# Performance work log

Hardware: AMD Instinct MI355X
Metric: run time of the kernel (lower is better)

Reference implementation:

```python
import jax, jax.numpy as jnp
import numpy as np

B, T, D = 2, 2048, 2048
N, K, H = 16, 8, 128  # heads, kv heads, head_dim
F = 8192              # ffn hidden


def _apply_rope(x, positions, max_wavelength=10000):
    # x: [B, L, heads, H]; positions: [B, L]
    half = x.shape[-1] // 2
    freq_exponents = (2.0 / x.shape[-1]) * jnp.arange(half, dtype=jnp.float32)
    timescale = max_wavelength ** freq_exponents
    radians = positions.astype(jnp.float32)[..., None] / timescale[None, None, :]
    radians = radians[..., None, :]  # [B, L, 1, half]
    sin, cos = jnp.sin(radians), jnp.cos(radians)
    x1, x2 = jnp.split(x, 2, axis=-1)
    return jnp.concatenate([x1 * cos - x2 * sin, x2 * cos + x1 * sin], axis=-1)


def _rms_norm(x, scale):
    var = jnp.mean(jnp.square(x), axis=-1, keepdims=True)
    return x * jax.lax.rsqrt(var + 1e-6) * (1 + scale)


def setup_inputs() -> dict:
    key = jax.random.key(0)
    ks = jax.random.split(key, 8)
    s = 0.02
    x = jax.random.normal(ks[0], (B, T, D), jnp.float32)
    positions = jnp.broadcast_to(jnp.arange(T, dtype=jnp.int32)[None, :], (B, T))
    causal = jnp.tril(jnp.ones((T, T), dtype=bool))
    attn_mask = jnp.broadcast_to(causal[None, None, :, :], (B, 1, T, T))
    return {
        "x": x,
        "positions": positions,
        "attn_mask": attn_mask,
        "w_q": jax.random.normal(ks[1], (N, D, H), jnp.float32) * s,
        "w_kv": jax.random.normal(ks[2], (2, K, D, H), jnp.float32) * s,
        "w_attn_vec": jax.random.normal(ks[3], (N, H, D), jnp.float32) * s,
        "scale_pre_attn": jax.random.normal(ks[4], (D,), jnp.float32) * s,
        "scale_pre_ffw": jax.random.normal(ks[5], (D,), jnp.float32) * s,
        "w_gating": jax.random.normal(ks[6], (2, D, F), jnp.float32) * s,
        "w_linear": jax.random.normal(ks[7], (F, D), jnp.float32) * s,
    }


def reference(x, positions, attn_mask, w_q, w_kv, w_attn_vec,
              scale_pre_attn, scale_pre_ffw, w_gating, w_linear):
    # pre-attention RMSNorm
    xn = _rms_norm(x, scale_pre_attn)

    # GQA projections
    q = jnp.einsum('BTD,NDH->BTNH', xn, w_q)
    kv = jnp.einsum('BSD,eKDH->eBSKH', xn, w_kv)
    k, v = kv[0], kv[1]

    q = _apply_rope(q, positions) * (H ** -0.5)
    k = _apply_rope(k, positions)

    G = N // K
    q = q.reshape(q.shape[0], q.shape[1], K, G, H)  # B T K G H
    logits = jnp.einsum('BTKGH,BSKH->BKGTS', q, k).astype(jnp.float32)
    big_neg = -2.3819763e38
    masked = jnp.where(attn_mask[:, :, None, :, :], logits, big_neg)
    probs = jax.nn.softmax(masked, axis=-1).astype(k.dtype)
    enc = jnp.einsum('BKGTS,BSKH->BTKGH', probs, v)
    enc = enc.reshape(enc.shape[0], enc.shape[1], N, H)
    attn_out = jnp.einsum('BTNH,NHD->BTD', enc, w_attn_vec)

    # residual + pre-FFN RMSNorm + GeGLU FFN
    residual = x + attn_out
    h = _rms_norm(residual, scale_pre_ffw)
    gate = jax.nn.gelu(jnp.dot(h, w_gating[0]))
    act = gate * jnp.dot(h, w_gating[1])
    out = residual + jnp.dot(act, w_linear)
    return out
```

## Files before the change

### kernel.cpp

```cpp
#include <hip/hip_runtime.h>
#include <hip/hip_bf16.h>


typedef __attribute__((ext_vector_type(8))) short bf16x8;
typedef __attribute__((ext_vector_type(4))) float f32x4;

#define GLP(p) ((const __attribute__((address_space(1))) void*)(p))
#define LDSP(p) ((__attribute__((address_space(3))) void*)(p))
#define FBAR() do { asm volatile("" ::: "memory"); __builtin_amdgcn_s_barrier(); asm volatile("" ::: "memory"); } while (0)

__device__ __forceinline__ float bf2f(unsigned short h) {
  union { unsigned int u; float f; } v; v.u = ((unsigned int)h) << 16; return v.f;
}
__device__ __forceinline__ unsigned short f2bf(float f) {
  union { float f; unsigned int u; } v; v.f = f;
  unsigned int r = v.u + 0x7fffu + ((v.u >> 16) & 1u);
  return (unsigned short)(r >> 16);
}
__device__ __forceinline__ float gelu_f(float x) {
  float t = tanhf(0.7978845608028654f * (x + 0.044715f * x * x * x));
  return 0.5f * x * (1.f + t);
}

template <int IN_F32>
__global__ __launch_bounds__(256) void rmsnorm_kernel(const void* __restrict__ x_,
                                                      const float* __restrict__ scale,
                                                      unsigned short* __restrict__ out) {
  int row = blockIdx.x, tid = threadIdx.x;
  float f[8]; float ss = 0.f;
  if (IN_F32) {
    const float* xr = (const float*)x_ + (size_t)row * 2048 + tid * 8;
#pragma unroll
    for (int i = 0; i < 8; ++i) { f[i] = xr[i]; ss += f[i] * f[i]; }
  } else {
    const unsigned short* xr = (const unsigned short*)x_ + (size_t)row * 2048;
    bf16x8 xv = *(const bf16x8*)(xr + tid * 8);
#pragma unroll
    for (int i = 0; i < 8; ++i) { f[i] = bf2f((unsigned short)xv[i]); ss += f[i] * f[i]; }
  }
#pragma unroll
  for (int off = 32; off >= 1; off >>= 1) ss += __shfl_xor(ss, off);
  __shared__ float red[4];
  if ((tid & 63) == 0) red[tid >> 6] = ss;
  __syncthreads();
  ss = red[0] + red[1] + red[2] + red[3];
  float r = rsqrtf(ss * (1.f / 2048.f) + 1e-6f);
  const float* sv = scale + tid * 8;
  bf16x8 o;
#pragma unroll
  for (int i = 0; i < 8; ++i) o[i] = (short)f2bf(f[i] * r * (1.f + sv[i]));
  *(bf16x8*)(out + (size_t)row * 2048 + tid * 8) = o;
}

__global__ __launch_bounds__(256) void transpose_cast_kernel(const float* __restrict__ in,
                                                             unsigned short* __restrict__ out,
                                                             int R, int ldi, long ibs, long obs) {
  __shared__ float tile[32][33];
  int z = blockIdx.z;
  const float* ip = in + (size_t)z * ibs;
  unsigned short* op = out + (size_t)z * obs;
  int c0 = blockIdx.x * 32, r0 = blockIdx.y * 32;
  int tx = threadIdx.x, ty = threadIdx.y;
#pragma unroll
  for (int i = 0; i < 32; i += 8)
    tile[ty + i][tx] = ip[(size_t)(r0 + ty + i) * ldi + (c0 + tx)];
  __syncthreads();
#pragma unroll
  for (int i = 0; i < 32; i += 8)
    op[(size_t)(c0 + ty + i) * R + (r0 + tx)] = f2bf(tile[tx][ty + i]);
}

__global__ __launch_bounds__(256) void vtrans_kernel(const unsigned short* __restrict__ qkv,
                                                     unsigned short* __restrict__ vT) {
  __shared__ unsigned short tile[32][33];
  int z = blockIdx.z, bb = z >> 3, kh = z & 7;
  int s0 = blockIdx.x * 32, h0 = blockIdx.y * 32;
  int tx = threadIdx.x, ty = threadIdx.y;
  const unsigned short* ip = qkv + ((size_t)bb * 2048) * 4096 + 3072 + kh * 128;
  unsigned short* op = vT + (size_t)z * 128 * 2048;
#pragma unroll
  for (int i = 0; i < 32; i += 8)
    tile[ty + i][tx] = ip[(size_t)(s0 + ty + i) * 4096 + h0 + tx];
  __syncthreads();
#pragma unroll
  for (int i = 0; i < 32; i += 8)
    op[(size_t)(h0 + ty + i) * 2048 + s0 + tx] = tile[tx][ty + i];
}

template <int BM, int MODE, int OUT_F32, int ADD_F32>
__global__ __launch_bounds__(512, 2) void gemm8p(const unsigned short* __restrict__ A,
                                                 const unsigned short* __restrict__ BT,
                                                 int Kd, int ldc, int gx,
                                                 void* __restrict__ out_,
                                                 const void* __restrict__ add_) {
  constexpr int MR = BM / 32;
  constexpr int MH = MR / 2;
  constexpr int ASZ = BM * 64;
  constexpr int BSZ = 256 * 64;
  __shared__ unsigned short lds[2 * ASZ + 2 * BSZ];
  unsigned short* aBuf0 = lds;
  unsigned short* aBuf1 = lds + ASZ;
  unsigned short* bBuf0 = lds + 2 * ASZ;
  unsigned short* bBuf1 = lds + 2 * ASZ + BSZ;

  int tid = threadIdx.x;
  int lane = tid & 63, w = tid >> 6;
  int quad = lane >> 4, l16 = lane & 15;
  int wm = w >> 2, wn = w & 3;
  int l8 = lane >> 3;

  int nwg = gridDim.x;
  int id = blockIdx.x;
  int swzid = (id & 7) * (nwg >> 3) + (id >> 3);
  int bx = swzid % gx, by = swzid / gx;
  long rowBase = (long)by * BM, colBase = (long)bx * 256;

  int csw = ((lane & 7) ^ l8) * 8;
  int rwB = (w >> 2) * 64 + (w & 3) * 8 + l8;
  int rwA = (BM == 256) ? (w * 8 + l8) : rwB;
  const unsigned short* aSrc = A + (rowBase + rwA) * (size_t)Kd + csw;
  const unsigned short* bSrc = BT + (colBase + rwB) * (size_t)Kd + csw;

  auto stgA = [&](unsigned short* dst, int h, int tt) {
    if (BM == 256) {
      __builtin_amdgcn_global_load_lds(GLP(aSrc + (size_t)(h * 64) * Kd + (size_t)tt * 64),
                                       LDSP(dst + (h * 128 + w * 8) * 64), 16, 0, 0);
      __builtin_amdgcn_global_load_lds(GLP(aSrc + (size_t)(128 + h * 64) * Kd + (size_t)tt * 64),
                                       LDSP(dst + (h * 128 + 64 + w * 8) * 64), 16, 0, 0);
    } else {
      __builtin_amdgcn_global_load_lds(GLP(aSrc + (size_t)(h * 32) * Kd + (size_t)tt * 64),
                                       LDSP(dst + (h * 64 + w * 8) * 64), 16, 0, 0);
    }
  };
  auto stgB = [&](unsigned short* dst, int h, int tt) {
    __builtin_amdgcn_global_load_lds(GLP(bSrc + (size_t)(h * 32) * Kd + (size_t)tt * 64),
                                     LDSP(dst + (h * 128 + w * 8) * 64), 16, 0, 0);
    __builtin_amdgcn_global_load_lds(GLP(bSrc + (size_t)(128 + h * 32) * Kd + (size_t)tt * 64),
                                     LDSP(dst + (h * 128 + 64 + w * 8) * 64), 16, 0, 0);
  };

  int swq0 = (quad * 8) ^ ((l16 & 7) * 8);
  int swq1 = (32 + quad * 8) ^ ((l16 & 7) * 8);
  auto rdA = [&](const unsigned short* cur, int i, int kk) -> bf16x8 {
    int rho = (BM == 256) ? ((i >> 2) * 128 + wm * 64 + (i & 3) * 16 + l16)
                          : ((i >> 1) * 64 + wm * 32 + (i & 1) * 16 + l16);
    return *(const bf16x8*)(cur + rho * 64 + (kk ? swq1 : swq0));
  };
  auto rdB = [&](const unsigned short* cur, int j, int kk) -> bf16x8 {
    int rho = (j >> 1) * 128 + wn * 32 + (j & 1) * 16 + l16;
    return *(const bf16x8*)(cur + rho * 64 + (kk ? swq1 : swq0));
  };

  f32x4 acc[MR][4];
#pragma unroll
  for (int i = 0; i < MR; ++i)
#pragma unroll
    for (int j = 0; j < 4; ++j) acc[i][j] = (f32x4){0.f, 0.f, 0.f, 0.f};

  stgA(aBuf0, 0, 0); stgB(bBuf0, 0, 0); stgB(bBuf0, 1, 0); stgA(aBuf0, 1, 0);
  stgA(aBuf1, 0, 1); stgB(bBuf1, 0, 1);
  if constexpr (BM == 256) asm volatile("s_waitcnt vmcnt(4)" ::: "memory");
  else                     asm volatile("s_waitcnt vmcnt(3)" ::: "memory");
  FBAR();

  int NT = Kd >> 6;
  bf16x8 af[MH][2], bfr0[2][2], bfr1[2][2];
  for (int t = 0; t < NT; ++t) {
    unsigned short* aCur = (t & 1) ? aBuf1 : aBuf0;
    unsigned short* bCur = (t & 1) ? bBuf1 : bBuf0;
    unsigned short* aNxt = (t & 1) ? aBuf0 : aBuf1;
    unsigned short* bNxt = (t & 1) ? bBuf0 : bBuf1;

#pragma unroll
    for (int i = 0; i < MH; ++i) { af[i][0] = rdA(aCur, i, 0); af[i][1] = rdA(aCur, i, 1); }
#pragma unroll
    for (int j = 0; j < 2; ++j) { bfr0[j][0] = rdB(bCur, j, 0); bfr0[j][1] = rdB(bCur, j, 1); }
    if (t + 1 < NT) stgB(bNxt, 1, t + 1);
    FBAR();
    __builtin_amdgcn_s_setprio(1);
#pragma unroll
    for (int kk = 0; kk < 2; ++kk)
#pragma unroll
      for (int i = 0; i < MH; ++i)
#pragma unroll
        for (int j = 0; j < 2; ++j)
          acc[i][j] = __builtin_amdgcn_mfma_f32_16x16x32_bf16(af[i][kk], bfr0[j][kk], acc[i][j], 0, 0, 0);
    __builtin_amdgcn_s_setprio(0);

#pragma unroll
    for (int j = 0; j < 2; ++j) { bfr1[j][0] = rdB(bCur, j + 2, 0); bfr1[j][1] = rdB(bCur, j + 2, 1); }
    if (t + 1 < NT) stgA(aNxt, 1, t + 1);
    FBAR();
    __builtin_amdgcn_s_setprio(1);
#pragma unroll
    for (int kk = 0; kk < 2; ++kk)
#pragma unroll
      for (int i = 0; i < MH; ++i)
#pragma unroll
        for (int j = 0; j < 2; ++j)
          acc[i][j + 2] = __builtin_amdgcn_mfma_f32_16x16x32_bf16(af[i][kk], bfr1[j][kk], acc[i][j + 2], 0, 0, 0);
    __builtin_amdgcn_s_setprio(0);

#pragma unroll
    for (int i = 0; i < MH; ++i) { af[i][0] = rdA(aCur, MH + i, 0); af[i][1] = rdA(aCur, MH + i, 1); }
    if (t + 2 < NT) stgA(aCur, 0, t + 2);
    FBAR();
    __builtin_amdgcn_s_setprio(1);
#pragma unroll
    for (int kk = 0; kk < 2; ++kk)
#pragma unroll
      for (int i = 0; i < MH; ++i)
#pragma unroll
        for (int j = 0; j < 2; ++j)
          acc[MH + i][j] = __builtin_amdgcn_mfma_f32_16x16x32_bf16(af[i][kk], bfr0[j][kk], acc[MH + i][j], 0, 0, 0);
    __builtin_amdgcn_s_setprio(0);

    if (t + 2 < NT) {
      stgB(bCur, 0, t + 2);
      if constexpr (BM == 256) asm volatile("s_waitcnt vmcnt(4)" ::: "memory");
      else                     asm volatile("s_waitcnt vmcnt(3)" ::: "memory");
    } else {
      asm volatile("s_waitcnt vmcnt(0)" ::: "memory");
    }
    FBAR();
    __builtin_amdgcn_s_setprio(1);
#pragma unroll
    for (int kk = 0; kk < 2; ++kk)
#pragma unroll
      for (int i = 0; i < MH; ++i)
#pragma unroll
        for (int j = 0; j < 2; ++j)
          acc[MH + i][j + 2] = __builtin_amdgcn_mfma_f32_16x16x32_bf16(af[i][kk], bfr1[j][kk], acc[MH + i][j + 2], 0, 0, 0);
    __builtin_amdgcn_s_setprio(0);
  }

  float* outf = (float*)out_;
  unsigned short* outb = (unsigned short*)out_;
  const float* addf = (const float*)add_;
  const unsigned short* addb = (const unsigned short*)add_;
  long orow = rowBase + wm * (BM / 2);
  long ocol = colBase + wn * 64 + l16;
#pragma unroll
  for (int i = 0; i < MR; ++i)
#pragma unroll
    for (int j = 0; j < 4; ++j)
#pragma unroll
      for (int rr = 0; rr < 4; ++rr) {
        long row = orow + i * 16 + quad * 4 + rr;
        long col = ocol + j * 16;
        long idx = row * (long)ldc + col;
        float v = acc[i][j][rr];
        if (MODE == 0) {
          outb[idx] = f2bf(v);
        } else if (MODE == 1) {
          v += (ADD_F32 ? addf[idx] : bf2f(addb[idx]));
          if (OUT_F32) outf[idx] = v; else outb[idx] = f2bf(v);
        } else {
          outb[idx] = f2bf(gelu_f(v) * bf2f(outb[idx]));
        }
      }
}

__global__ __launch_bounds__(256) void rope_kernel(unsigned short* __restrict__ qkv,
                                                   const int* __restrict__ pos) {
  int gid = blockIdx.x * 256 + threadIdx.x;
  int hp = gid & 63;
  int rh = gid >> 6;
  int row = rh / 24;
  int head = rh - row * 24;
  float p = (float)pos[row];
  long cb; float sc;
  if (head < 16) { cb = (long)head * 128; sc = 0.08838834764831845f; }
  else { cb = 2048 + (long)(head - 16) * 128; sc = 1.f; }
  unsigned short* ptr = qkv + (long)row * 4096 + cb;
  float inv = exp2f(-(float)hp * (13.287712379549449f / 64.f));
  float ang = p * inv;
  float s = sinf(ang), c = cosf(ang);
  float x1 = bf2f(ptr[hp]), x2 = bf2f(ptr[hp + 64]);
  ptr[hp]      = f2bf((x1 * c - x2 * s) * sc);
  ptr[hp + 64] = f2bf((x2 * c + x1 * s) * sc);
}

__global__ __launch_bounds__(256, 2) void attn_kernel(const unsigned short* __restrict__ qkv,
                                                      const unsigned short* __restrict__ vT,
                                                      unsigned short* __restrict__ enc) {
  extern __shared__ char smem[];
  unsigned short* sK = (unsigned short*)smem;
  unsigned short* sVT = sK + 64 * 128;
  float* sS = (float*)(smem + 32768);
  unsigned short* sP = (unsigned short*)(smem + 32768 + 16896);
  float* sM = (float*)(smem + 32768 + 16896 + 9216);
  float* sL = sM + 64;
  float* sAl = sL + 64;

  int qt = blockIdx.x, n = blockIdx.y, b = blockIdx.z;
  int tid = threadIdx.x, lane = tid & 63, w = tid >> 6;
  int quad = lane >> 4, l16 = lane & 15;
  int kh = n >> 1;
  long rowQ = (long)b * 2048 + (long)qt * 64;

  bf16x8 qf[4];
  {
    const unsigned short* qp = qkv + (rowQ + w * 16 + l16) * 4096 + n * 128 + quad * 8;
#pragma unroll
    for (int ks = 0; ks < 4; ++ks) qf[ks] = *(const bf16x8*)(qp + ks * 32);
  }
  if (tid < 64) { sM[tid] = -1e30f; sL[tid] = 0.f; }
  f32x4 oacc[8];
#pragma unroll
  for (int t = 0; t < 8; ++t) oacc[t] = (f32x4){0.f, 0.f, 0.f, 0.f};

  int srow = tid >> 2, cg = tid & 3;

  for (int st = 0; st <= qt; ++st) {
    __syncthreads();
#pragma unroll
    for (int it = 0; it < 4; ++it) {
      int idx = it * 256 + tid;
      int r = idx >> 4, c = idx & 15;
      bf16x8 kv8 = *(const bf16x8*)(qkv + ((long)b * 2048 + st * 64 + r) * 4096 + 2048 + kh * 128 + c * 8);
      *(bf16x8*)(sK + r * 128 + ((c ^ (r & 7)) * 8)) = kv8;
    }
#pragma unroll
    for (int it = 0; it < 4; ++it) {
      int idx = it * 256 + tid;
      int h = idx >> 3, c = idx & 7;
      bf16x8 vv8 = *(const bf16x8*)(vT + ((long)(b * 8 + kh) * 128 + h) * 2048 + st * 64 + c * 8);
      *(bf16x8*)(sVT + h * 64 + ((c ^ (h & 7)) * 8)) = vv8;
    }
    __syncthreads();

    f32x4 sacc[4];
#pragma unroll
    for (int nt = 0; nt < 4; ++nt) sacc[nt] = (f32x4){0.f, 0.f, 0.f, 0.f};
#pragma unroll
    for (int ks = 0; ks < 4; ++ks)
#pragma unroll
      for (int nt = 0; nt < 4; ++nt) {
        int r = nt * 16 + l16;
        bf16x8 kf = *(const bf16x8*)(sK + r * 128 + (((ks * 4 + quad) ^ (r & 7)) * 8));
        sacc[nt] = __builtin_amdgcn_mfma_f32_16x16x32_bf16(qf[ks], kf, sacc[nt], 0, 0, 0);
      }
#pragma unroll
    for (int nt = 0; nt < 4; ++nt)
#pragma unroll
      for (int r = 0; r < 4; ++r)
        sS[(w * 16 + quad * 4 + r) * 66 + nt * 16 + l16] = sacc[nt][r];
    __syncthreads();

    float vals[16];
    int tglob = qt * 64 + srow;
    float mx = -1e30f;
#pragma unroll
    for (int j = 0; j < 16; ++j) {
      int col = cg * 16 + j;
      float v = sS[srow * 66 + col];
      if (st * 64 + col > tglob) v = -1e30f;
      vals[j] = v;
      mx = fmaxf(mx, v);
    }
    mx = fmaxf(mx, __shfl_xor(mx, 1));
    mx = fmaxf(mx, __shfl_xor(mx, 2));
    float m_old = sM[srow], l_old = sL[srow];
    float m_new = fmaxf(m_old, mx);
    float alpha = __expf(m_old - m_new);
    float sum = 0.f;
#pragma unroll
    for (int j = 0; j < 16; ++j) { vals[j] = __expf(vals[j] - m_new); sum += vals[j]; }
    sum += __shfl_xor(sum, 1);
    sum += __shfl_xor(sum, 2);
    float l_new = alpha * l_old + sum;
    __syncthreads();

#pragma unroll
    for (int jj = 0; jj < 8; ++jj) {
      unsigned int pk = (unsigned int)f2bf(vals[2 * jj]) | ((unsigned int)f2bf(vals[2 * jj + 1]) << 16);
      *(unsigned int*)(sP + srow * 72 + cg * 16 + jj * 2) = pk;
    }
    if (cg == 0) { sM[srow] = m_new; sL[srow] = l_new; sAl[srow] = alpha; }
    __syncthreads();

#pragma unroll
    for (int r = 0; r < 4; ++r) {
      float al = sAl[w * 16 + quad * 4 + r];
#pragma unroll
      for (int nt = 0; nt < 8; ++nt) oacc[nt][r] *= al;
    }
#pragma unroll
    for (int ks = 0; ks < 2; ++ks) {
      bf16x8 pf = *(const bf16x8*)(sP + (w * 16 + l16) * 72 + ks * 32 + quad * 8);
#pragma unroll
      for (int nt = 0; nt < 8; ++nt) {
        int hh = nt * 16 + l16;
        bf16x8 vf = *(const bf16x8*)(sVT + hh * 64 + (((ks * 4 + quad) ^ (hh & 7)) * 8));
        oacc[nt] = __builtin_amdgcn_mfma_f32_16x16x32_bf16(pf, vf, oacc[nt], 0, 0, 0);
      }
    }
  }

#pragma unroll
  for (int r = 0; r < 4; ++r) {
    float invl = 1.f / sL[w * 16 + quad * 4 + r];
    long trow = rowQ + w * 16 + quad * 4 + r;
#pragma unroll
    for (int nt = 0; nt < 8; ++nt)
      enc[trow * 2048 + n * 128 + nt * 16 + l16] = f2bf(oacc[nt][r] * invl);
  }
}

extern "C" void kernel_launch(void* const* d_in, const int* in_sizes, int n_in,
                              void* d_out, int out_size, void* d_ws, size_t ws_size,
                              hipStream_t stream) {
  const float* x = (const float*)d_in[0];
  const int* positions = (const int*)d_in[1];
  const float* wq = (const float*)d_in[3];
  const float* wkv = (const float*)d_in[4];
  const float* wav = (const float*)d_in[5];
  const float* s_attn = (const float*)d_in[6];
  const float* s_ffw = (const float*)d_in[7];
  const float* wg = (const float*)d_in[8];
  const float* wl = (const float*)d_in[9];
  float* outp = (float*)d_out;

  char* ws = (char*)d_ws;
  size_t o = 0;
  unsigned short* XN = (unsigned short*)(ws + o);    o += (size_t)4096 * 2048 * 2;
  unsigned short* WQKVT = (unsigned short*)(ws + o); o += (size_t)4096 * 2048 * 2;
  unsigned short* WAVT = (unsigned short*)(ws + o);  o += (size_t)2048 * 2048 * 2;
  unsigned short* WGT = (unsigned short*)(ws + o);   o += (size_t)8192 * 2048 * 2;
  unsigned short* QKV = (unsigned short*)(ws + o);   o += (size_t)4096 * 4096 * 2;
  unsigned short* VTb = (unsigned short*)(ws + o);   o += (size_t)16 * 128 * 2048 * 2;
  unsigned short* ACT = (unsigned short*)(ws + o);   o += (size_t)4096 * 8192 * 2;
  unsigned short* ENC = WQKVT;
  unsigned short* RES = QKV;
  unsigned short* HB = XN;

  dim3 b256(256), bT(32, 8);

  rmsnorm_kernel<1><<<4096, b256, 0, stream>>>(x, s_attn, XN);

  transpose_cast_kernel<<<dim3(4, 64, 16), bT, 0, stream>>>(wq, WQKVT, 2048, 128, 262144L, 262144L);
  transpose_cast_kernel<<<dim3(4, 64, 8), bT, 0, stream>>>(wkv, WQKVT + (size_t)2048 * 2048, 2048, 128, 262144L, 262144L);
  transpose_cast_kernel<<<dim3(4, 64, 8), bT, 0, stream>>>(wkv + (size_t)8 * 262144, WQKVT + (size_t)3072 * 2048, 2048, 128, 262144L, 262144L);
  transpose_cast_kernel<<<dim3(64, 64, 1), bT, 0, stream>>>(wav, WAVT, 2048, 2048, 0L, 0L);

  gemm8p<256, 0, 0, 0><<<256, 512, 0, stream>>>(XN, WQKVT, 2048, 4096, 16, QKV, nullptr);

  vtrans_kernel<<<dim3(64, 4, 16), bT, 0, stream>>>(QKV, VTb);

  rope_kernel<<<24576, b256, 0, stream>>>(QKV, positions);

  attn_kernel<<<dim3(32, 16, 2), b256, 59648, stream>>>(QKV, VTb, ENC);

  gemm8p<128, 1, 0, 1><<<256, 512, 0, stream>>>(ENC, WAVT, 2048, 2048, 8, RES, x);

  rmsnorm_kernel<0><<<4096, b256, 0, stream>>>(RES, s_ffw, HB);

  for (int half = 0; half < 2; ++half) {
    long f0 = (long)half * 4096;
    transpose_cast_kernel<<<dim3(128, 64, 1), bT, 0, stream>>>(wg + f0, WGT, 2048, 8192, 0L, 0L);
    transpose_cast_kernel<<<dim3(128, 64, 1), bT, 0, stream>>>(wg + (size_t)2048 * 8192 + f0,
                                                               WGT + (size_t)4096 * 2048, 2048, 8192, 0L, 0L);
    gemm8p<256, 0, 0, 0><<<256, 512, 0, stream>>>(HB, WGT + (size_t)4096 * 2048, 2048, 8192, 16, ACT + f0, nullptr);
    gemm8p<256, 2, 0, 0><<<256, 512, 0, stream>>>(HB, WGT, 2048, 8192, 16, ACT + f0, nullptr);
  }

  transpose_cast_kernel<<<dim3(64, 256, 1), bT, 0, stream>>>(wl, WGT, 8192, 2048, 0L, 0L);
  gemm8p<128, 1, 1, 0><<<256, 512, 0, stream>>>(ACT, WGT, 8192, 2048, 8, outp, RES);
}
```

Before: 1.062 ms.

## Restructure GEMM load/compute pipeline waits and reverse attention query-tile order

Reorganizes the GEMM main loop's global-to-LDS staging. Loads for the next tiles are issued in pairs earlier in the loop, the vmcnt waits are recomputed, explicit lgkmcnt(0) waits with sched barriers go before each MFMA block, and the third and fourth MFMA groups are merged under a single barrier. The intent is to keep more loads in flight and overlap them better with MFMA work. The attention kernel now processes query tiles in reverse order so the heaviest causal tiles launch first, which should improve load balance. The new wait counts and extra barriers risk pipeline stalls or correctness issues if the counts are wrong.

```diff
diff --git a/kernel.cpp b/kernel.cpp
--- a/kernel.cpp
+++ b/kernel.cpp
@@ -8,6 +8,7 @@
 #define GLP(p) ((const __attribute__((address_space(1))) void*)(p))
 #define LDSP(p) ((__attribute__((address_space(3))) void*)(p))
 #define FBAR() do { asm volatile("" ::: "memory"); __builtin_amdgcn_s_barrier(); asm volatile("" ::: "memory"); } while (0)
+#define LGKM0() do { asm volatile("s_waitcnt lgkmcnt(0)" ::: "memory"); __builtin_amdgcn_sched_barrier(0); } while (0)
 
 __device__ __forceinline__ float bf2f(unsigned short h) {
   union { unsigned int u; float f; } v; v.u = ((unsigned int)h) << 16; return v.f;
@@ -157,13 +158,14 @@
 #pragma unroll
     for (int j = 0; j < 4; ++j) acc[i][j] = (f32x4){0.f, 0.f, 0.f, 0.f};
 
-  stgA(aBuf0, 0, 0); stgB(bBuf0, 0, 0); stgB(bBuf0, 1, 0); stgA(aBuf0, 1, 0);
+  int NT = Kd >> 6;
+  stgA(aBuf0, 0, 0); stgB(bBuf0, 0, 0);
+  stgB(bBuf0, 1, 0); stgA(aBuf0, 1, 0);
   stgA(aBuf1, 0, 1); stgB(bBuf1, 0, 1);
-  if constexpr (BM == 256) asm volatile("s_waitcnt vmcnt(4)" ::: "memory");
-  else                     asm volatile("s_waitcnt vmcnt(3)" ::: "memory");
+  if constexpr (BM == 256) asm volatile("s_waitcnt vmcnt(8)" ::: "memory");
+  else                     asm volatile("s_waitcnt vmcnt(6)" ::: "memory");
   FBAR();
 
-  int NT = Kd >> 6;
   bf16x8 af[MH][2], bfr0[2][2], bfr1[2][2];
   for (int t = 0; t < NT; ++t) {
     unsigned short* aCur = (t & 1) ? aBuf1 : aBuf0;
@@ -175,8 +177,9 @@
     for (int i = 0; i < MH; ++i) { af[i][0] = rdA(aCur, i, 0); af[i][1] = rdA(aCur, i, 1); }
 #pragma unroll
     for (int j = 0; j < 2; ++j) { bfr0[j][0] = rdB(bCur, j, 0); bfr0[j][1] = rdB(bCur, j, 1); }
-    if (t + 1 < NT) stgB(bNxt, 1, t + 1);
+    if (t + 1 < NT) { stgB(bNxt, 1, t + 1); stgA(aNxt, 1, t + 1); }
     FBAR();
+    LGKM0();
     __builtin_amdgcn_s_setprio(1);
 #pragma unroll
     for (int kk = 0; kk < 2; ++kk)
@@ -186,11 +189,20 @@
         for (int j = 0; j < 2; ++j)
           acc[i][j] = __builtin_amdgcn_mfma_f32_16x16x32_bf16(af[i][kk], bfr0[j][kk], acc[i][j], 0, 0, 0);
     __builtin_amdgcn_s_setprio(0);
+    if (t + 1 < NT) {
+      if constexpr (BM == 256) asm volatile("s_waitcnt vmcnt(10)" ::: "memory");
+      else                     asm volatile("s_waitcnt vmcnt(7)" ::: "memory");
+    } else {
+      if constexpr (BM == 256) asm volatile("s_waitcnt vmcnt(2)" ::: "memory");
+      else                     asm volatile("s_waitcnt vmcnt(1)" ::: "memory");
+    }
+    FBAR();
 
 #pragma unroll
     for (int j = 0; j < 2; ++j) { bfr1[j][0] = rdB(bCur, j + 2, 0); bfr1[j][1] = rdB(bCur, j + 2, 1); }
-    if (t + 1 < NT) stgA(aNxt, 1, t + 1);
+    if (t + 2 < NT) { stgA(aCur, 0, t + 2); stgB(bCur, 0, t + 2); }
     FBAR();
+    LGKM0();
     __builtin_amdgcn_s_setprio(1);
 #pragma unroll
     for (int kk = 0; kk < 2; ++kk)
@@ -200,11 +212,21 @@
         for (int j = 0; j < 2; ++j)
           acc[i][j + 2] = __builtin_amdgcn_mfma_f32_16x16x32_bf16(af[i][kk], bfr1[j][kk], acc[i][j + 2], 0, 0, 0);
     __builtin_amdgcn_s_setprio(0);
+    if (t + 2 < NT) {
+      if constexpr (BM == 256) asm volatile("s_waitcnt vmcnt(12)" ::: "memory");
+      else                     asm volatile("s_waitcnt vmcnt(9)" ::: "memory");
+    } else if (t + 1 < NT) {
+      if constexpr (BM == 256) asm volatile("s_waitcnt vmcnt(8)" ::: "memory");
+      else                     asm volatile("s_waitcnt vmcnt(6)" ::: "memory");
+    } else {
+      asm volatile("s_waitcnt vmcnt(0)" ::: "memory");
+    }
+    FBAR();
 
 #pragma unroll
     for (int i = 0; i < MH; ++i) { af[i][0] = rdA(aCur, MH + i, 0); af[i][1] = rdA(aCur, MH + i, 1); }
-    if (t + 2 < NT) stgA(aCur, 0, t + 2);
     FBAR();
+    LGKM0();
     __builtin_amdgcn_s_setprio(1);
 #pragma unroll
     for (int kk = 0; kk < 2; ++kk)
@@ -213,17 +235,6 @@
 #pragma unroll
         for (int j = 0; j < 2; ++j)
           acc[MH + i][j] = __builtin_amdgcn_mfma_f32_16x16x32_bf16(af[i][kk], bfr0[j][kk], acc[MH + i][j], 0, 0, 0);
-    __builtin_amdgcn_s_setprio(0);
-
-    if (t + 2 < NT) {
-      stgB(bCur, 0, t + 2);
-      if constexpr (BM == 256) asm volatile("s_waitcnt vmcnt(4)" ::: "memory");
-      else                     asm volatile("s_waitcnt vmcnt(3)" ::: "memory");
-    } else {
-      asm volatile("s_waitcnt vmcnt(0)" ::: "memory");
-    }
-    FBAR();
-    __builtin_amdgcn_s_setprio(1);
 #pragma unroll
     for (int kk = 0; kk < 2; ++kk)
 #pragma unroll
@@ -232,6 +243,16 @@
         for (int j = 0; j < 2; ++j)
           acc[MH + i][j + 2] = __builtin_amdgcn_mfma_f32_16x16x32_bf16(af[i][kk], bfr1[j][kk], acc[MH + i][j + 2], 0, 0, 0);
     __builtin_amdgcn_s_setprio(0);
+    if (t + 1 < NT) {
+      if (t + 2 < NT) {
+        if constexpr (BM == 256) asm volatile("s_waitcnt vmcnt(8)" ::: "memory");
+        else                     asm volatile("s_waitcnt vmcnt(6)" ::: "memory");
+      } else {
+        if constexpr (BM == 256) asm volatile("s_waitcnt vmcnt(4)" ::: "memory");
+        else                     asm volatile("s_waitcnt vmcnt(3)" ::: "memory");
+      }
+      FBAR();
+    }
   }
 
   float* outf = (float*)out_;
@@ -293,7 +314,7 @@
   float* sL = sM + 64;
   float* sAl = sL + 64;
 
-  int qt = blockIdx.x, n = blockIdx.y, b = blockIdx.z;
+  int qt = (int)gridDim.x - 1 - blockIdx.x, n = blockIdx.y, b = blockIdx.z;
   int tid = threadIdx.x, lane = tid & 63, w = tid >> 6;
   int quad = lane >> 4, l16 = lane & 15;
   int kh = n >> 1;
```

Measured after the change: 1.109 ms. +4.4%, slower.

## Keep attention softmax state in registers and reverse causal tile order

Applied to the files above, without the earlier changes.

The online softmax now works directly on the MFMA accumulator fragments. Row max and row sum are reduced with lane shuffles, and the running max and sum live in per-thread registers. This removes the fp32 score staging buffer in LDS, the shared max/sum/alpha arrays and three block barriers per key tile. Shared memory per block shrinks and the launch bound rises to 3 blocks per CU. Query tiles are also issued longest-first to balance the causal workload. The P buffer row stride of 68 elements leaves the 16-byte fragment reads misaligned, which could split or slow those LDS loads.

```diff
diff --git a/kernel.cpp b/kernel.cpp
--- a/kernel.cpp
+++ b/kernel.cpp
@@ -281,19 +281,15 @@
   ptr[hp + 64] = f2bf((x2 * c + x1 * s) * sc);
 }
 
-__global__ __launch_bounds__(256, 2) void attn_kernel(const unsigned short* __restrict__ qkv,
+__global__ __launch_bounds__(256, 3) void attn_kernel(const unsigned short* __restrict__ qkv,
                                                       const unsigned short* __restrict__ vT,
                                                       unsigned short* __restrict__ enc) {
   extern __shared__ char smem[];
   unsigned short* sK = (unsigned short*)smem;
   unsigned short* sVT = sK + 64 * 128;
-  float* sS = (float*)(smem + 32768);
-  unsigned short* sP = (unsigned short*)(smem + 32768 + 16896);
-  float* sM = (float*)(smem + 32768 + 16896 + 9216);
-  float* sL = sM + 64;
-  float* sAl = sL + 64;
-
-  int qt = blockIdx.x, n = blockIdx.y, b = blockIdx.z;
+  unsigned short* sP = sVT + 64 * 128;
+
+  int qt = (int)gridDim.x - 1 - blockIdx.x, n = blockIdx.y, b = blockIdx.z;
   int tid = threadIdx.x, lane = tid & 63, w = tid >> 6;
   int quad = lane >> 4, l16 = lane & 15;
   int kh = n >> 1;
@@ -305,12 +301,12 @@
 #pragma unroll
     for (int ks = 0; ks < 4; ++ks) qf[ks] = *(const bf16x8*)(qp + ks * 32);
   }
-  if (tid < 64) { sM[tid] = -1e30f; sL[tid] = 0.f; }
   f32x4 oacc[8];
 #pragma unroll
   for (int t = 0; t < 8; ++t) oacc[t] = (f32x4){0.f, 0.f, 0.f, 0.f};
-
-  int srow = tid >> 2, cg = tid & 3;
+  float m_r[4], l_r[4];
+#pragma unroll
+  for (int r = 0; r < 4; ++r) { m_r[r] = -1e30f; l_r[r] = 0.f; }
 
   for (int st = 0; st <= qt; ++st) {
     __syncthreads();
@@ -341,54 +337,47 @@
         bf16x8 kf = *(const bf16x8*)(sK + r * 128 + (((ks * 4 + quad) ^ (r & 7)) * 8));
         sacc[nt] = __builtin_amdgcn_mfma_f32_16x16x32_bf16(qf[ks], kf, sacc[nt], 0, 0, 0);
       }
+
+    float p[4][4];
+#pragma unroll
+    for (int r = 0; r < 4; ++r) {
+      int qrow = w * 16 + quad * 4 + r;
+      float mx = -1e30f;
+#pragma unroll
+      for (int nt = 0; nt < 4; ++nt) {
+        float v = sacc[nt][r];
+        if (st * 64 + nt * 16 + l16 > qt * 64 + qrow) v = -1e30f;
+        p[nt][r] = v;
+        mx = fmaxf(mx, v);
+      }
+      mx = fmaxf(mx, __shfl_xor(mx, 1));
+      mx = fmaxf(mx, __shfl_xor(mx, 2));
+      mx = fmaxf(mx, __shfl_xor(mx, 4));
+      mx = fmaxf(mx, __shfl_xor(mx, 8));
+      float m_new = fmaxf(m_r[r], mx);
+      float al = __expf(m_r[r] - m_new);
+      float sum = 0.f;
+#pragma unroll
+      for (int nt = 0; nt < 4; ++nt) { p[nt][r] = __expf(p[nt][r] - m_new); sum += p[nt][r]; }
+      sum += __shfl_xor(sum, 1);
+      sum += __shfl_xor(sum, 2);
+      sum += __shfl_xor(sum, 4);
+      sum += __shfl_xor(sum, 8);
+      l_r[r] = al * l_r[r] + sum;
+      m_r[r] = m_new;
+#pragma unroll
+      for (int nt = 0; nt < 8; ++nt) oacc[nt][r] *= al;
+    }
+
 #pragma unroll
     for (int nt = 0; nt < 4; ++nt)
 #pragma unroll
       for (int r = 0; r < 4; ++r)
-        sS[(w * 16 + quad * 4 + r) * 66 + nt * 16 + l16] = sacc[nt][r];
-    __syncthreads();
-
-    float vals[16];
-    int tglob = qt * 64 + srow;
-    float mx = -1e30f;
-#pragma unroll
-    for (int j = 0; j < 16; ++j) {
-      int col = cg * 16 + j;
-      float v = sS[srow * 66 + col];
-      if (st * 64 + col > tglob) v = -1e30f;
-      vals[j] = v;
-      mx = fmaxf(mx, v);
-    }
-    mx = fmaxf(mx, __shfl_xor(mx, 1));
-    mx = fmaxf(mx, __shfl_xor(mx, 2));
-    float m_old = sM[srow], l_old = sL[srow];
-    float m_new = fmaxf(m_old, mx);
-    float alpha = __expf(m_old - m_new);
-    float sum = 0.f;
-#pragma unroll
-    for (int j = 0; j < 16; ++j) { vals[j] = __expf(vals[j] - m_new); sum += vals[j]; }
-    sum += __shfl_xor(sum, 1);
-    sum += __shfl_xor(sum, 2);
-    float l_new = alpha * l_old + sum;
-    __syncthreads();
-
-#pragma unroll
-    for (int jj = 0; jj < 8; ++jj) {
-      unsigned int pk = (unsigned int)f2bf(vals[2 * jj]) | ((unsigned int)f2bf(vals[2 * jj + 1]) << 16);
-      *(unsigned int*)(sP + srow * 72 + cg * 16 + jj * 2) = pk;
-    }
-    if (cg == 0) { sM[srow] = m_new; sL[srow] = l_new; sAl[srow] = alpha; }
-    __syncthreads();
-
-#pragma unroll
-    for (int r = 0; r < 4; ++r) {
-      float al = sAl[w * 16 + quad * 4 + r];
-#pragma unroll
-      for (int nt = 0; nt < 8; ++nt) oacc[nt][r] *= al;
-    }
+        sP[(w * 16 + quad * 4 + r) * 68 + nt * 16 + l16] = f2bf(p[nt][r]);
+
 #pragma unroll
     for (int ks = 0; ks < 2; ++ks) {
-      bf16x8 pf = *(const bf16x8*)(sP + (w * 16 + l16) * 72 + ks * 32 + quad * 8);
+      bf16x8 pf = *(const bf16x8*)(sP + (w * 16 + l16) * 68 + ks * 32 + quad * 8);
 #pragma unroll
       for (int nt = 0; nt < 8; ++nt) {
         int hh = nt * 16 + l16;
@@ -400,7 +389,7 @@
 
 #pragma unroll
   for (int r = 0; r < 4; ++r) {
-    float invl = 1.f / sL[w * 16 + quad * 4 + r];
+    float invl = 1.f / l_r[r];
     long trow = rowQ + w * 16 + quad * 4 + r;
 #pragma unroll
     for (int nt = 0; nt < 8; ++nt)
@@ -450,7 +439,7 @@
 
   rope_kernel<<<24576, b256, 0, stream>>>(QKV, positions);
 
-  attn_kernel<<<dim3(32, 16, 2), b256, 59648, stream>>>(QKV, VTb, ENC);
+  attn_kernel<<<dim3(32, 16, 2), b256, 41472, stream>>>(QKV, VTb, ENC);
 
   gemm8p<128, 1, 0, 1><<<256, 512, 0, stream>>>(ENC, WAVT, 2048, 2048, 8, RES, x);
 
```

Result: no change. 1.064 ms (+0.2%).
